# Kernel optimization log

Measured on AMD Instinct MI355X. Metric: run time of the kernel, lower is better.

The kernel has to match this reference:

```python
import jax, jax.numpy as jnp
import numpy as np

B, N, F, UNITS = 8, 2048, 64, 64

def setup_inputs() -> dict:
    key = jax.random.key(0)
    ks = jax.random.split(key, 7)
    inputs = jax.random.normal(ks[0], (B, N, F), dtype=jnp.float32)
    Dynamic_L = jax.random.normal(ks[1], (B, N, N), dtype=jnp.float32)
    W = jax.random.uniform(ks[2], (B, N, N, 3), dtype=jnp.float32)
    Geo = jax.random.normal(ks[3], (N, N), dtype=jnp.float32)
    KL = jax.random.normal(ks[4], (N, N), dtype=jnp.float32)
    # Dense(Units, tanh) params (glorot-ish scale)
    Wd = jax.random.normal(ks[5], (F, UNITS), dtype=jnp.float32) / np.sqrt(F)
    bd = jnp.zeros((UNITS,), dtype=jnp.float32)
    return {"inputs": inputs, "Dynamic_L": Dynamic_L, "W": W,
            "Geo": Geo, "KL": KL, "Wd": Wd, "bd": bd}

def reference(inputs, Dynamic_L, W, Geo, KL, Wd, bd):
    # Weighted fusion of three N x N matrices; Geo/KL broadcast over batch.
    Fusion = Dynamic_L * W[..., 0] + Geo[None] * W[..., 1] + KL[None] * W[..., 2]  # [B,N,N]
    Fusion = jax.nn.softmax(Fusion, axis=-1)
    G1 = jnp.einsum('bnm,bmf->bnf', Fusion, inputs)  # graph matmul [B,N,F]
    return jnp.tanh(G1 @ Wd + bd)  # Dense(Units, tanh) -> [B,N,UNITS]
```

## Files before the change

kernel.cpp:

```cpp
#include <hip/hip_runtime.h>
#include <hip/hip_fp16.h>

#define Nn 2048
#define Ff 64
#define Uu 64
#define NT 256
#define NCH 64
#define G1S 68

typedef _Float16 f16x2 __attribute__((ext_vector_type(2)));
typedef _Float16 f16x8 __attribute__((ext_vector_type(8)));
typedef float    f32x4 __attribute__((ext_vector_type(4)));

#define MFMA32(a,b,c) __builtin_amdgcn_mfma_f32_16x16x32_f16(a,b,c,0,0,0)
#define GLD16(gp, lp) __builtin_amdgcn_global_load_lds(                      \
    (const __attribute__((address_space(1))) void*)(gp),                     \
    (__attribute__((address_space(3))) void*)(lp), 16, 0, 0)

#define OD0 0
#define OD1 2048
#define OG  4096
#define OK  6144
#define OW0 8192
#define OW1 14336
#define STG 20480
#define OP   40960
#define OG1A 45056
#define OG1B 49408
#define OWS  53760
#define OINV 53888
#define SMSZ 54016

__global__ __launch_bounds__(256) void transposeX(const float* __restrict__ X,
                                                  _Float16* __restrict__ Xt) {
    __shared__ _Float16 tile[64][65];
    const int b = blockIdx.x, kt = blockIdx.y;
    #pragma unroll
    for (int i = 0; i < 16; ++i) {
        int e  = i * 256 + threadIdx.x;
        int kk = e >> 6, ff = e & 63;
        tile[ff][kk] = (_Float16)X[((size_t)b * Nn + kt * 64 + kk) * Ff + ff];
    }
    __syncthreads();
    #pragma unroll
    for (int i = 0; i < 16; ++i) {
        int e  = i * 256 + threadIdx.x;
        int ff = e >> 6, kk = e & 63;
        Xt[((size_t)b * Ff + ff) * Nn + kt * 64 + kk] = tile[ff][kk];
    }
}

__global__ __launch_bounds__(NT, 2) void fused_gcn(
    const _Float16* __restrict__ Xt,
    const float* __restrict__ Dyn,
    const float* __restrict__ Wf,
    const float* __restrict__ Geo,
    const float* __restrict__ KLm,
    const float* __restrict__ Wd,
    const float* __restrict__ bdv,
    float* __restrict__ out)
{
    __shared__ __align__(16) char SM[SMSZ];

    const int t    = threadIdx.x;
    const int lane = t & 63;
    const int wid  = t >> 6;
    const int r    = lane & 15;
    const int kg   = lane >> 4;
    const int gidx = blockIdx.x & 127;
    const int p    = blockIdx.x >> 7;
    const int n0   = gidx << 4;
    const int b0   = p * 2, b1 = p * 2 + 1;

    const char* dyn0 = (const char*)(Dyn + ((size_t)b0 * Nn + n0) * Nn);
    const char* dyn1 = (const char*)(Dyn + ((size_t)b1 * Nn + n0) * Nn);
    const char* geo  = (const char*)(Geo + (size_t)n0 * Nn);
    const char* klm  = (const char*)(KLm + (size_t)n0 * Nn);
    const char* wf0  = (const char*)(Wf + ((size_t)b0 * Nn + n0) * (size_t)Nn * 3);
    const char* wf1  = (const char*)(Wf + ((size_t)b1 * Nn + n0) * (size_t)Nn * 3);

    const size_t dA = (size_t)(lane >> 3) * (Nn * 4) + (size_t)(lane & 7) * 16;
    const size_t dB = dA + (size_t)8 * (Nn * 4);
#define WL(j) ((size_t)(((j)*1024 + lane*16) / 384) * (Nn*12) + (size_t)(((j)*1024 + lane*16) % 384))

    const char *s0, *s1, *s2, *s3, *s4;
    int l0, l1, l2, l3, l4, i0, i1, i2, i3, i4;
    if (wid == 0) {
        s0 = dyn0 + dA;   l0 = OD0;        i0 = 128;
        s1 = dyn0 + dB;   l1 = OD0 + 1024; i1 = 128;
        s2 = dyn1 + dA;   l2 = OD1;        i2 = 128;
        s3 = dyn1 + dB;   l3 = OD1 + 1024; i3 = 128;
        s4 = geo  + dA;   l4 = OG;         i4 = 128;
    } else if (wid == 1) {
        s0 = geo + dB;    l0 = OG + 1024;  i0 = 128;
        s1 = klm + dA;    l1 = OK;         i1 = 128;
        s2 = klm + dB;    l2 = OK + 1024;  i2 = 128;
        s3 = wf0 + WL(0); l3 = OW0;        i3 = 384;
        s4 = wf0 + WL(1); l4 = OW0 + 1024; i4 = 384;
    } else if (wid == 2) {
        s0 = wf0 + WL(2); l0 = OW0 + 2048; i0 = 384;
        s1 = wf0 + WL(3); l1 = OW0 + 3072; i1 = 384;
        s2 = wf0 + WL(4); l2 = OW0 + 4096; i2 = 384;
        s3 = wf0 + WL(5); l3 = OW0 + 5120; i3 = 384;
        s4 = wf1 + WL(0); l4 = OW1;        i4 = 384;
    } else {
        s0 = wf1 + WL(1); l0 = OW1 + 1024; i0 = 384;
        s1 = wf1 + WL(2); l1 = OW1 + 2048; i1 = 384;
        s2 = wf1 + WL(3); l2 = OW1 + 3072; i2 = 384;
        s3 = wf1 + WL(4); l3 = OW1 + 4096; i3 = 384;
        s4 = wf1 + WL(5); l4 = OW1 + 5120; i4 = 384;
    }

#define STAGE(P) { char* _b = SM + (P) * STG;                         \
    GLD16(s0, _b + l0); GLD16(s1, _b + l1); GLD16(s2, _b + l2);       \
    GLD16(s3, _b + l3); GLD16(s4, _b + l4);                           \
    s0 += i0; s1 += i1; s2 += i2; s3 += i3; s4 += i4; }

    const _Float16* xw0 = Xt + (size_t)b0 * Ff * Nn
                        + (size_t)(wid * 16 + r) * Nn + (kg << 3);
    const _Float16* xw1 = Xt + (size_t)b1 * Ff * Nn
                        + (size_t)(wid * 16 + r) * Nn + (kg << 3);

    const int e = t >> 4, q = t & 15;
    f32x4 acc0 = {0.f,0.f,0.f,0.f}, acc1 = {0.f,0.f,0.f,0.f};
    float rs0 = 0.f, rs1 = 0.f;

    STAGE(0);
    asm volatile("s_waitcnt vmcnt(0)" ::: "memory");
    __builtin_amdgcn_s_barrier();

    #pragma unroll 1
    for (int c = 0; c < NCH; ++c) {
        const int pc = c & 1;

        f16x8 bf0 = *(const f16x8*)xw0;
        f16x8 bf1 = *(const f16x8*)xw1;
        xw0 += 32; xw1 += 32;
        __builtin_amdgcn_sched_barrier(0);
        if (c + 1 < NCH) STAGE(pc ^ 1);
        __builtin_amdgcn_sched_barrier(0);

        {
            const char* st = SM + pc * STG;
            const float* Dc0 = (const float*)(st + OD0);
            const float* Dc1 = (const float*)(st + OD1);
            const float* Gc  = (const float*)(st + OG);
            const float* Kc  = (const float*)(st + OK);
            const float* Wc0 = (const float*)(st + OW0);
            const float* Wc1 = (const float*)(st + OW1);
            float2 gv = *(const float2*)(Gc + e * 32 + q * 2);
            float2 kv = *(const float2*)(Kc + e * 32 + q * 2);
            float2 d0 = *(const float2*)(Dc0 + e * 32 + q * 2);
            float2 d1 = *(const float2*)(Dc1 + e * 32 + q * 2);
            float2 wa0 = *(const float2*)(Wc0 + e * 96 + q * 6);
            float2 wb0 = *(const float2*)(Wc0 + e * 96 + q * 6 + 2);
            float2 wc0 = *(const float2*)(Wc0 + e * 96 + q * 6 + 4);
            float2 wa1 = *(const float2*)(Wc1 + e * 96 + q * 6);
            float2 wb1 = *(const float2*)(Wc1 + e * 96 + q * 6 + 2);
            float2 wc1 = *(const float2*)(Wc1 + e * 96 + q * 6 + 4);
            float e00 = __expf(fminf(d0.x*wa0.x + gv.x*wa0.y + kv.x*wb0.x, 11.f));
            float e01 = __expf(fminf(d0.y*wb0.y + gv.y*wc0.x + kv.y*wc0.y, 11.f));
            float e10 = __expf(fminf(d1.x*wa1.x + gv.x*wa1.y + kv.x*wb1.x, 11.f));
            float e11 = __expf(fminf(d1.y*wb1.y + gv.y*wc1.x + kv.y*wc1.y, 11.f));
            _Float16 h00 = (_Float16)e00, h01 = (_Float16)e01;
            _Float16 h10 = (_Float16)e10, h11 = (_Float16)e11;
            rs0 += (float)h00 + (float)h01;
            rs1 += (float)h10 + (float)h11;
            char* Pb = SM + OP + pc * 2048;
            const int pa = (e * 64 + q * 4) ^ ((e & 7) << 4);
            f16x2 v0 = {h00, h01}, v1 = {h10, h11};
            *(f16x2*)(Pb + pa) = v0;
            *(f16x2*)(Pb + 1024 + pa) = v1;
        }
        asm volatile("s_waitcnt lgkmcnt(0)" ::: "memory");
        __builtin_amdgcn_sched_barrier(0);
        __builtin_amdgcn_s_barrier();

        {
            const char* Pc = SM + OP + pc * 2048;
            const int ao = (r * 64 + kg * 16) ^ ((r & 7) << 4);
            f16x8 af0 = *(const f16x8*)(Pc + ao);
            f16x8 af1 = *(const f16x8*)(Pc + 1024 + ao);
            acc0 = MFMA32(af0, bf0, acc0);
            acc1 = MFMA32(af1, bf1, acc1);
        }
        asm volatile("s_waitcnt vmcnt(0)" ::: "memory");
        __builtin_amdgcn_sched_barrier(0);
        __builtin_amdgcn_s_barrier();
    }

    float v0 = rs0, v1 = rs1;
    v0 += __shfl_xor(v0, 1, 64); v0 += __shfl_xor(v0, 2, 64);
    v0 += __shfl_xor(v0, 4, 64); v0 += __shfl_xor(v0, 8, 64);
    v1 += __shfl_xor(v1, 1, 64); v1 += __shfl_xor(v1, 2, 64);
    v1 += __shfl_xor(v1, 4, 64); v1 += __shfl_xor(v1, 8, 64);
    float* ws = (float*)(SM + OWS);
    if ((lane & 15) == 0) {
        ws[(wid << 2) + (lane >> 4)] = v0;
        ws[16 + (wid << 2) + (lane >> 4)] = v1;
    }
    __syncthreads();
    float* inv = (float*)(SM + OINV);
    if (t < 32) inv[t] = 1.0f / ws[t];
    __syncthreads();

    float* g1a = (float*)(SM + OG1A);
    float* g1b = (float*)(SM + OG1B);
    #pragma unroll
    for (int i = 0; i < 4; ++i) {
        const int ro = (kg << 2) + i;
        g1a[ro * G1S + (wid << 4) + r] = acc0[i] * inv[ro];
        g1b[ro * G1S + (wid << 4) + r] = acc1[i] * inv[16 + ro];
    }
    __syncthreads();

    const int row0 = wid << 2;
    const float* ga = g1a + row0 * G1S;
    const float* gb = g1b + row0 * G1S;
    float bb = bdv[lane];
    float a0 = bb, a1 = bb, a2 = bb, a3 = bb;
    float c0 = bb, c1 = bb, c2 = bb, c3 = bb;
    #pragma unroll 4
    for (int f = 0; f < Ff; ++f) {
        float wdv = Wd[f * Uu + lane];
        a0 += ga[f] * wdv;           a1 += ga[G1S + f] * wdv;
        a2 += ga[2 * G1S + f] * wdv; a3 += ga[3 * G1S + f] * wdv;
        c0 += gb[f] * wdv;           c1 += gb[G1S + f] * wdv;
        c2 += gb[2 * G1S + f] * wdv; c3 += gb[3 * G1S + f] * wdv;
    }
    float oa[4] = {a0, a1, a2, a3}, ob[4] = {c0, c1, c2, c3};
    #pragma unroll
    for (int i = 0; i < 4; ++i) {
        float x  = fminf(fmaxf(oa[i], -15.f), 15.f);
        float ex = __expf(2.f * x);
        out[((size_t)b0 * Nn + n0 + row0 + i) * Uu + lane] = (ex - 1.f) / (ex + 1.f);
        float y  = fminf(fmaxf(ob[i], -15.f), 15.f);
        float ey = __expf(2.f * y);
        out[((size_t)b1 * Nn + n0 + row0 + i) * Uu + lane] = (ey - 1.f) / (ey + 1.f);
    }
}

extern "C" void kernel_launch(void* const* d_in, const int* in_sizes, int n_in,
                              void* d_out, int out_size, void* d_ws, size_t ws_size,
                              hipStream_t stream) {
    const float* X   = (const float*)d_in[0];
    const float* Dyn = (const float*)d_in[1];
    const float* Wf  = (const float*)d_in[2];
    const float* Geo = (const float*)d_in[3];
    const float* KLm = (const float*)d_in[4];
    const float* Wd  = (const float*)d_in[5];
    const float* bdv = (const float*)d_in[6];
    float* out = (float*)d_out;

    _Float16* Xt = (_Float16*)d_ws;
    transposeX<<<dim3(8, Nn / 64), dim3(256), 0, stream>>>(X, Xt);
    fused_gcn<<<dim3(4 * 128), dim3(NT), 0, stream>>>(
        Xt, Dyn, Wf, Geo, KLm, Wd, bdv, out);
}
```

Baseline: 135.5 us.

## Triple-buffer global-to-LDS staging and prefetch X fragments one chunk ahead

Moves the LDS staging of D/G/K/W tiles from double to triple buffering, so two chunks are in flight while the current one is consumed. The X operand fragments are also register-prefetched one iteration ahead, and the end-of-iteration full vmcnt(0) wait becomes a partial wait with explicit counts. This hides global load latency behind the exp/MFMA work. In exchange LDS use grows from about 54KB to 74KB per block, which may cut occupancy, and the hand-counted vmcnt values must match the real number of outstanding loads.

```diff
diff --git a/kernel.cpp b/kernel.cpp
--- a/kernel.cpp
+++ b/kernel.cpp
@@ -24,12 +24,12 @@
 #define OW0 8192
 #define OW1 14336
 #define STG 20480
-#define OP   40960
-#define OG1A 45056
-#define OG1B 49408
-#define OWS  53760
-#define OINV 53888
-#define SMSZ 54016
+#define OP   61440
+#define OG1A 65536
+#define OG1B 69888
+#define OWS  74240
+#define OINV 74368
+#define SMSZ 74496
 
 __global__ __launch_bounds__(256) void transposeX(const float* __restrict__ X,
                                                   _Float16* __restrict__ Xt) {
@@ -111,7 +111,7 @@
         s4 = wf1 + WL(5); l4 = OW1 + 5120; i4 = 384;
     }
 
-#define STAGE(P) { char* _b = SM + (P) * STG;                         \
+#define STAGE(BUFI) { char* _b = SM + (BUFI) * STG;                   \
     GLD16(s0, _b + l0); GLD16(s1, _b + l1); GLD16(s2, _b + l2);       \
     GLD16(s3, _b + l3); GLD16(s4, _b + l4);                           \
     s0 += i0; s1 += i1; s2 += i2; s3 += i3; s4 += i4; }
@@ -126,22 +126,32 @@
     float rs0 = 0.f, rs1 = 0.f;
 
     STAGE(0);
-    asm volatile("s_waitcnt vmcnt(0)" ::: "memory");
+    STAGE(1);
+    f16x8 bfc0 = *(const f16x8*)xw0;
+    f16x8 bfc1 = *(const f16x8*)xw1;
+    xw0 += 32; xw1 += 32;
+    asm volatile("s_waitcnt vmcnt(7)" ::: "memory");
+    __builtin_amdgcn_sched_barrier(0);
     __builtin_amdgcn_s_barrier();
 
+    int pcur = 0;
     #pragma unroll 1
     for (int c = 0; c < NCH; ++c) {
-        const int pc = c & 1;
-
-        f16x8 bf0 = *(const f16x8*)xw0;
-        f16x8 bf1 = *(const f16x8*)xw1;
-        xw0 += 32; xw1 += 32;
-        __builtin_amdgcn_sched_barrier(0);
-        if (c + 1 < NCH) STAGE(pc ^ 1);
+        const int pc2 = c & 1;
+
+        f16x8 bfn0, bfn1;
+        if (c + 1 < NCH) {
+            bfn0 = *(const f16x8*)xw0;
+            bfn1 = *(const f16x8*)xw1;
+            xw0 += 32; xw1 += 32;
+        }
+        __builtin_amdgcn_sched_barrier(0);
+        if (c + 2 < NCH) { const int pst = (pcur + 2 >= 3) ? pcur - 1 : pcur + 2;
+                           STAGE(pst); }
         __builtin_amdgcn_sched_barrier(0);
 
         {
-            const char* st = SM + pc * STG;
+            const char* st = SM + pcur * STG;
             const float* Dc0 = (const float*)(st + OD0);
             const float* Dc1 = (const float*)(st + OD1);
             const float* Gc  = (const float*)(st + OG);
@@ -166,27 +176,36 @@
             _Float16 h10 = (_Float16)e10, h11 = (_Float16)e11;
             rs0 += (float)h00 + (float)h01;
             rs1 += (float)h10 + (float)h11;
-            char* Pb = SM + OP + pc * 2048;
+            char* Pbuf = SM + OP + pc2 * 2048;
             const int pa = (e * 64 + q * 4) ^ ((e & 7) << 4);
             f16x2 v0 = {h00, h01}, v1 = {h10, h11};
-            *(f16x2*)(Pb + pa) = v0;
-            *(f16x2*)(Pb + 1024 + pa) = v1;
+            *(f16x2*)(Pbuf + pa) = v0;
+            *(f16x2*)(Pbuf + 1024 + pa) = v1;
         }
         asm volatile("s_waitcnt lgkmcnt(0)" ::: "memory");
         __builtin_amdgcn_sched_barrier(0);
         __builtin_amdgcn_s_barrier();
 
         {
-            const char* Pc = SM + OP + pc * 2048;
+            const char* Pc = SM + OP + pc2 * 2048;
             const int ao = (r * 64 + kg * 16) ^ ((r & 7) << 4);
             f16x8 af0 = *(const f16x8*)(Pc + ao);
             f16x8 af1 = *(const f16x8*)(Pc + 1024 + ao);
-            acc0 = MFMA32(af0, bf0, acc0);
-            acc1 = MFMA32(af1, bf1, acc1);
-        }
-        asm volatile("s_waitcnt vmcnt(0)" ::: "memory");
+            acc0 = MFMA32(af0, bfc0, acc0);
+            acc1 = MFMA32(af1, bfc1, acc1);
+        }
+        bfc0 = bfn0; bfc1 = bfn1;
+
+        __builtin_amdgcn_sched_barrier(0);
+        if (c + 2 < NCH) {
+            asm volatile("s_waitcnt vmcnt(9)" ::: "memory");
+        } else if (c + 1 < NCH) {
+            asm volatile("s_waitcnt vmcnt(4)" ::: "memory");
+        }
         __builtin_amdgcn_sched_barrier(0);
         __builtin_amdgcn_s_barrier();
+
+        pcur = (pcur == 2) ? 0 : pcur + 1;
     }
 
     float v0 = rs0, v1 = rs1;
```

After: 142.1 us. 1.05x slower.
